# Kernel optimization log

Measured on AMD Instinct MI355X. Metric: run time of the kernel, lower is better.

## Reference

```python
import jax, jax.numpy as jnp
import numpy as np

B, S, HID, NH = 4, 4096, 1024, 16
D = HID // NH                 # head_dim = 64
WIN, CHUNK = 512, 128
CPW = WIN // CHUNK            # chunks_per_window = 4
NW = S // WIN                 # num windows = 8
NC = S // CHUNK               # num chunks = 32
SCALE = D ** -0.5             # head_dim_scaling


def setup_inputs() -> dict:
    key = jax.random.key(0)
    k = jax.random.split(key, 8)
    hidden_states = jax.random.normal(k[0], (B, S, HID), jnp.float32)
    init = lambda kk: jax.random.normal(kk, (HID, HID), jnp.float32) * (HID ** -0.5)
    Wq, Wk, Wv, Wo = init(k[1]), init(k[2]), init(k[3]), init(k[4])
    # nn.Parameter(randn(1,H,1,1,D).clamp(-1,1) * head_dim_scaling)
    adaptive_mu_k = jnp.clip(jax.random.normal(k[5], (1, NH, 1, 1, D), jnp.float32), -1.0, 1.0) * SCALE
    adaptive_phi = jnp.clip(jax.random.normal(k[6], (1, NH, 1, 1, D), jnp.float32), -1.0, 1.0) * SCALE
    # RoPE tables, (1,1,S,D) to broadcast against (B,H,S,D)
    inv_freq = 1.0 / (10000.0 ** (jnp.arange(0, D, 2, dtype=jnp.float32) / D))
    freqs = jnp.einsum('s,f->sf', jnp.arange(S, dtype=jnp.float32), inv_freq)
    emb = jnp.concatenate([freqs, freqs], axis=-1)  # (S, D)
    cos = jnp.cos(emb)[None, None]
    sin = jnp.sin(emb)[None, None]
    return dict(hidden_states=hidden_states, Wq=Wq, Wk=Wk, Wv=Wv, Wo=Wo,
                adaptive_mu_k=adaptive_mu_k, adaptive_phi=adaptive_phi, cos=cos, sin=sin)


def rotate_half(x):
    x1, x2 = jnp.split(x, 2, axis=-1)
    return jnp.concatenate([-x2, x1], axis=-1)


def reference(hidden_states, Wq, Wk, Wv, Wv_unused=None, **_ignored):
    raise NotImplementedError  # replaced below


def _eva_forward(hidden_states, Wq, Wk, Wv, Wo, adaptive_mu_k, adaptive_phi, cos, sin):
    b, s, _ = hidden_states.shape
    def proj(W):  # nn.Linear(bias=False): x @ W.T, then (b,s,H,D)->(b,H,s,D)
        return jnp.einsum('bse,de->bsd', hidden_states, W).reshape(b, s, NH, D).transpose(0, 2, 1, 3)
    q, kt, v = proj(Wq), proj(Wk), proj(Wv)
    q = q * cos + rotate_half(q) * sin
    kt = kt * cos + rotate_half(kt) * sin

    # ---- eva_prep_kv_func: per-chunk control-variate summaries ----
    kc = kt.reshape(b, NH, NC, CHUNK, D)
    vc = v.reshape(b, NH, NC, CHUNK, D)
    mu = adaptive_mu_k.reshape(NH, D)
    phi = adaptive_phi.reshape(NH, D)
    # prm-projection logits: scale*<param,k> - scale*||k||^2/2
    norm = SCALE * 0.5 * jnp.sum(kc * kc, axis=-1)                      # (b,h,c,j)
    beta = jax.nn.softmax(SCALE * jnp.einsum('bhcjd,hd->bhcj', kc, mu) - norm, axis=-1)
    gamma = jax.nn.softmax(SCALE * jnp.einsum('bhcjd,hd->bhcj', kc, phi) - norm, axis=-1)
    rfa_k = jnp.einsum('bhcj,bhcjd->bhcd', beta, kc)                    # (b,h,NC,D)
    rfa_v = jnp.einsum('bhcj,bhcjd->bhcd', gamma, vc)

    # ---- eva_agg_func: windowed exact attn + chunk-RFA attn, joint softmax ----
    qw = q.reshape(b, NH, NW, WIN, D)
    kw = kt.reshape(b, NH, NW, WIN, D)
    vw = v.reshape(b, NH, NW, WIN, D)
    win_scores = SCALE * jnp.einsum('bhwid,bhwjd->bhwij', qw, kw)
    neg = jnp.finfo(win_scores.dtype).min
    causal = jnp.tril(jnp.ones((WIN, WIN), bool))
    win_scores = jnp.where(causal[None, None, None], win_scores, neg)
    chunk_scores = SCALE * jnp.einsum('bhwid,bhcd->bhwic', qw, rfa_k)
    # queries in window w attend to chunk-RFAs of strictly earlier windows
    chunk_ok = (jnp.arange(NC)[None, :] // CPW) < jnp.arange(NW)[:, None]  # (NW,NC)
    chunk_scores = jnp.where(chunk_ok[None, None, :, None, :], chunk_scores, neg)
    attn = jax.nn.softmax(jnp.concatenate([win_scores, chunk_scores], axis=-1), axis=-1)
    out = (jnp.einsum('bhwij,bhwjd->bhwid', attn[..., :WIN], vw)
           + jnp.einsum('bhwic,bhcd->bhwid', attn[..., WIN:], rfa_v))
    out = out.reshape(b, NH, s, D).transpose(0, 2, 1, 3).reshape(b, s, HID)
    return jnp.einsum('bsd,ed->bse', out, Wo)  # o_proj


def reference(hidden_states, Wq, Wk, Wv, Wo, adaptive_mu_k, adaptive_phi, cos, sin):
    return _eva_forward(hidden_states, Wq, Wk, Wv, Wo, adaptive_mu_k, adaptive_phi, cos, sin)
```

## Files before the change

kernel.cpp:

```cpp
#include <hip/hip_runtime.h>
#include <hip/hip_bf16.h>
#include <stdint.h>

#define SCALE_ 0.125f
#define K_L2E 0.18033688f

typedef __bf16 bf16x8 __attribute__((ext_vector_type(8)));
typedef float f32x4 __attribute__((ext_vector_type(4)));
typedef unsigned short us8v __attribute__((ext_vector_type(8)));
typedef unsigned int u32x2 __attribute__((ext_vector_type(2)));

__device__ __forceinline__ unsigned short f2bf(float f) {
  unsigned int u = __builtin_bit_cast(unsigned int, f);
  u += 0x7fffu + ((u >> 16) & 1u);
  return (unsigned short)(u >> 16);
}
__device__ __forceinline__ float bf2f(unsigned short h) {
  unsigned int u = ((unsigned int)h) << 16;
  return __builtin_bit_cast(float, u);
}
__device__ __forceinline__ unsigned short f2bf_n(float f) {
  __bf16 b = (__bf16)f;
  return __builtin_bit_cast(unsigned short, b);
}
__device__ __forceinline__ unsigned packbf(float lo, float hi) {
  return (unsigned)f2bf_n(lo) | ((unsigned)f2bf_n(hi) << 16);
}
__device__ __forceinline__ float exp2_fast(float x) {
  return __builtin_amdgcn_exp2f(x);
}
__device__ __forceinline__ f32x4 mfma16(bf16x8 a, bf16x8 b, f32x4 c) {
  return __builtin_amdgcn_mfma_f32_16x16x32_bf16(a, b, c, 0, 0, 0);
}
__device__ __forceinline__ f32x4 max4(f32x4 a, f32x4 b) {
  f32x4 r;
  r[0] = fmaxf(a[0], b[0]); r[1] = fmaxf(a[1], b[1]);
  r[2] = fmaxf(a[2], b[2]); r[3] = fmaxf(a[3], b[3]);
  return r;
}
__device__ __forceinline__ void gl2lds16(const unsigned short* g, unsigned short* l) {
  __builtin_amdgcn_global_load_lds(
      (const __attribute__((address_space(1))) unsigned int*)g,
      (__attribute__((address_space(3))) unsigned int*)l, 16, 0, 0);
}

__global__ __launch_bounds__(256) void cvt_kernel(const float* __restrict__ src,
                                                  unsigned short* __restrict__ dst,
                                                  int n8) {
  int i = blockIdx.x * 256 + threadIdx.x;
  if (i >= n8) return;
  us8v o;
#pragma unroll
  for (int e = 0; e < 8; ++e) o[e] = f2bf(src[(size_t)i * 8 + e]);
  *(us8v*)(dst + (size_t)i * 8) = o;
}

template <int MODE>
__global__ __launch_bounds__(256, 2) void gemm_kernel(
    const unsigned short* __restrict__ A, const unsigned short* __restrict__ W0,
    const unsigned short* __restrict__ W1, const unsigned short* __restrict__ W2,
    unsigned short* __restrict__ Qb, unsigned short* __restrict__ Kb,
    unsigned short* __restrict__ VT, const float* __restrict__ cosT,
    const float* __restrict__ sinT, float* __restrict__ Out) {
  __shared__ unsigned short As[128 * 32];
  __shared__ unsigned short Bs[128 * 32];
  const int tid = threadIdx.x;
  const int lane = tid & 63, wv = tid >> 6;
  const int lr = lane & 15, lg = lane >> 4;
  const int wr = wv >> 1, wc = wv & 1;
  const int tm = blockIdx.x * 16 + (blockIdx.y >> 3);
  const int tn = blockIdx.y & 7;
  const int z = blockIdx.z;
  const unsigned short* Wp = (MODE == 1) ? W0 : (z == 0 ? W0 : (z == 1 ? W1 : W2));
  const unsigned short* Ab = A + (size_t)tm * 128 * 1024;
  const unsigned short* Wb = Wp + (size_t)tn * 128 * 1024;

  const int srow = tid >> 2;
  const int scol = (tid & 3) * 8;

  f32x4 zero = {0.f, 0.f, 0.f, 0.f};
  f32x4 acc[4][4];
#pragma unroll
  for (int i = 0; i < 4; ++i)
#pragma unroll
    for (int j = 0; j < 4; ++j) acc[i][j] = zero;

  for (int ks = 0; ks < 32; ++ks) {
    const int k0 = ks * 32;
    __syncthreads();
    gl2lds16(Ab + (size_t)srow * 1024 + k0 + scol, As + srow * 32 + scol);
    gl2lds16(Ab + (size_t)(64 + srow) * 1024 + k0 + scol, As + (64 + srow) * 32 + scol);
    gl2lds16(Wb + (size_t)srow * 1024 + k0 + scol, Bs + srow * 32 + scol);
    gl2lds16(Wb + (size_t)(64 + srow) * 1024 + k0 + scol, Bs + (64 + srow) * 32 + scol);
    __syncthreads();
    bf16x8 av[4], bv[4];
#pragma unroll
    for (int mt = 0; mt < 4; ++mt)
      av[mt] = *(const bf16x8*)(As + (wr * 64 + mt * 16 + lr) * 32 + lg * 8);
#pragma unroll
    for (int nt = 0; nt < 4; ++nt)
      bv[nt] = *(const bf16x8*)(Bs + (wc * 64 + nt * 16 + lr) * 32 + lg * 8);
    __builtin_amdgcn_s_setprio(1);
#pragma unroll
    for (int mt = 0; mt < 4; ++mt)
#pragma unroll
      for (int nt = 0; nt < 4; ++nt)
        acc[mt][nt] = mfma16(av[mt], bv[nt], acc[mt][nt]);
    __builtin_amdgcn_s_setprio(0);
  }

  if constexpr (MODE == 0) {
    if (z < 2) {
      unsigned short* Dst = (z == 0) ? Qb : Kb;
#pragma unroll
      for (int mt = 0; mt < 4; ++mt) {
#pragma unroll
        for (int r = 0; r < 4; ++r) {
          const int m = tm * 128 + wr * 64 + mt * 16 + lg * 4 + r;
          const int b = m >> 12, s = m & 4095;
#pragma unroll
          for (int nt = 0; nt < 4; ++nt) {
            const int n = tn * 128 + wc * 64 + nt * 16 + lr;
            const int h = n >> 6, d = n & 63;
            float v = acc[mt][nt][r];
            const float cs = cosT[s * 64 + d];
            const float sn = sinT[s * 64 + d];
            const float pv = acc[mt][nt ^ 2][r];
            v = v * cs + ((nt < 2) ? -pv : pv) * sn;
            Dst[((size_t)(b * 16 + h) * 4096 + s) * 64 + d] = f2bf_n(v);
          }
        }
      }
    } else {
#pragma unroll
      for (int mt = 0; mt < 4; ++mt) {
        const int m0 = tm * 128 + wr * 64 + mt * 16 + lg * 4;
        const int b = m0 >> 12, s0 = m0 & 4095;
#pragma unroll
        for (int nt = 0; nt < 4; ++nt) {
          const int n = tn * 128 + wc * 64 + nt * 16 + lr;
          const int h = n >> 6, d = n & 63;
          u32x2 pw;
          pw[0] = packbf(acc[mt][nt][0], acc[mt][nt][1]);
          pw[1] = packbf(acc[mt][nt][2], acc[mt][nt][3]);
          *(u32x2*)(VT + ((size_t)(b * 16 + h) * 64 + d) * 4096 + s0) = pw;
        }
      }
    }
  } else {
#pragma unroll
    for (int mt = 0; mt < 4; ++mt) {
#pragma unroll
      for (int r = 0; r < 4; ++r) {
        const int m = tm * 128 + wr * 64 + mt * 16 + lg * 4 + r;
#pragma unroll
        for (int nt = 0; nt < 4; ++nt) {
          const int n = tn * 128 + wc * 64 + nt * 16 + lr;
          Out[(size_t)m * 1024 + n] = acc[mt][nt][r];
        }
      }
    }
  }
}

__global__ __launch_bounds__(128) void prep_kernel(
    const unsigned short* __restrict__ Kb, const unsigned short* __restrict__ VT,
    const float* __restrict__ mu, const float* __restrict__ phi,
    unsigned short* __restrict__ rfaK, unsigned short* __restrict__ rfaVT) {
  __shared__ float kc[128][65];
  __shared__ float betaS[128], gammaS[128];
  __shared__ float red[8];
  const int tid = threadIdx.x, lane = tid & 63, wid = tid >> 6;
  const int bh = blockIdx.x >> 5, c = blockIdx.x & 31;
  const int h = bh & 15;
  const size_t rowbase = ((size_t)bh * 4096 + c * 128 + tid) * 64;

  float nn = 0.f, dmu = 0.f, dphi = 0.f;
#pragma unroll
  for (int d8 = 0; d8 < 8; ++d8) {
    us8v kv = *(const us8v*)(Kb + rowbase + d8 * 8);
#pragma unroll
    for (int e = 0; e < 8; ++e) {
      const int d = d8 * 8 + e;
      const float kf = bf2f(kv[e]);
      kc[tid][d] = kf;
      nn += kf * kf;
      dmu += kf * mu[h * 64 + d];
      dphi += kf * phi[h * 64 + d];
    }
  }
  const float lb = SCALE_ * dmu - 0.5f * SCALE_ * nn;
  const float lgm = SCALE_ * dphi - 0.5f * SCALE_ * nn;
  float mb = lb, mg = lgm;
  for (int off = 1; off < 64; off <<= 1) {
    mb = fmaxf(mb, __shfl_xor(mb, off));
    mg = fmaxf(mg, __shfl_xor(mg, off));
  }
  if (lane == 0) { red[wid * 2] = mb; red[wid * 2 + 1] = mg; }
  __syncthreads();
  mb = fmaxf(red[0], red[2]);
  mg = fmaxf(red[1], red[3]);
  const float eb = __expf(lb - mb), eg = __expf(lgm - mg);
  float sb = eb, sg = eg;
  for (int off = 1; off < 64; off <<= 1) {
    sb += __shfl_xor(sb, off);
    sg += __shfl_xor(sg, off);
  }
  if (lane == 0) { red[4 + wid * 2] = sb; red[4 + wid * 2 + 1] = sg; }
  betaS[tid] = eb;
  gammaS[tid] = eg;
  __syncthreads();
  sb = red[4] + red[6];
  sg = red[5] + red[7];

  if (tid < 64) {
    float a = 0.f;
    for (int j = 0; j < 128; ++j) a += betaS[j] * kc[j][tid];
    rfaK[((size_t)bh * 32 + c) * 64 + tid] = f2bf(a / sb);
    const unsigned short* vrow = VT + ((size_t)bh * 64 + tid) * 4096 + c * 128;
    float av = 0.f;
#pragma unroll
    for (int j8 = 0; j8 < 16; ++j8) {
      us8v vv = *(const us8v*)(vrow + j8 * 8);
#pragma unroll
      for (int e = 0; e < 8; ++e) av += gammaS[j8 * 8 + e] * bf2f(vv[e]);
    }
    rfaVT[((size_t)bh * 64 + tid) * 32 + c] = f2bf(av / sg);
  }
}

template <int NCT, bool HASA, bool MASKA, bool MASKB, bool CH>
__device__ __forceinline__ void attn_tile2(
    const unsigned short* __restrict__ ksrc, const unsigned short* __restrict__ vsrc,
    int t, int w, int qrA, int qrB, int lr, int lg, const bf16x8* qaA,
    const bf16x8* qaB, f32x4* oA, f32x4* oB, float& mA, float& lA, float& mB,
    float& lB, unsigned short (*__restrict__ PtA)[136],
    unsigned short (*__restrict__ PtB)[136]) {
  constexpr int VSTRIDE = CH ? 32 : 4096;
  constexpr int NKS = CH ? 1 : 4;
  bf16x8 vf[NKS * 4];
#pragma unroll
  for (int ks = 0; ks < NKS; ++ks)
#pragma unroll
    for (int dt = 0; dt < 4; ++dt)
      vf[ks * 4 + dt] =
          *(const bf16x8*)(vsrc + (size_t)(dt * 16) * VSTRIDE + ks * 32);
  f32x4 stA[NCT], stB[NCT];
#pragma unroll
  for (int ct = 0; ct < NCT; ++ct) {
    bf16x8 b0 = *(const bf16x8*)(ksrc + (ct * 16 + lr) * 64 + lg * 8);
    bf16x8 b1 = *(const bf16x8*)(ksrc + (ct * 16 + lr) * 64 + 32 + lg * 8);
    f32x4 sb_ = {0.f, 0.f, 0.f, 0.f};
    sb_ = mfma16(b0, qaB[0], sb_);
    sb_ = mfma16(b1, qaB[1], sb_);
    f32x4 sa_ = {0.f, 0.f, 0.f, 0.f};
    if constexpr (HASA) {
      sa_ = mfma16(b0, qaA[0], sa_);
      sa_ = mfma16(b1, qaA[1], sa_);
    }
#pragma unroll
    for (int r = 0; r < 4; ++r) {
      const int kidx = ct * 16 + lg * 4 + r;
      float svb = sb_[r] * K_L2E;
      if constexpr (CH) {
        if (kidx >= 4 * w) svb = -1e30f;
      } else if constexpr (MASKB) {
        if (t * 128 + kidx > qrB) svb = -1e30f;
      }
      sb_[r] = svb;
      if constexpr (HASA) {
        float sva = sa_[r] * K_L2E;
        if constexpr (CH) {
          if (kidx >= 4 * w) sva = -1e30f;
        } else if constexpr (MASKA) {
          if (t * 128 + kidx > qrA) sva = -1e30f;
        }
        sa_[r] = sva;
      }
    }
    stB[ct] = sb_;
    if constexpr (HASA) stA[ct] = sa_;
  }
  if constexpr (HASA) {
    f32x4 m4 = stA[0];
#pragma unroll
    for (int ct = 1; ct < NCT; ++ct) m4 = max4(m4, stA[ct]);
    float rm = fmaxf(fmaxf(m4[0], m4[1]), fmaxf(m4[2], m4[3]));
    rm = fmaxf(rm, __shfl_xor(rm, 16));
    rm = fmaxf(rm, __shfl_xor(rm, 32));
    const float mn = fmaxf(mA, rm);
    const float a = exp2_fast(mA - mn);
    f32x4 s4 = {0.f, 0.f, 0.f, 0.f};
#pragma unroll
    for (int ct = 0; ct < NCT; ++ct) {
#pragma unroll
      for (int r = 0; r < 4; ++r) stA[ct][r] = exp2_fast(stA[ct][r] - mn);
      s4 += stA[ct];
    }
    float rs = (s4[0] + s4[1]) + (s4[2] + s4[3]);
    rs += __shfl_xor(rs, 16);
    rs += __shfl_xor(rs, 32);
    lA = lA * a + rs;
    mA = mn;
#pragma unroll
    for (int dt = 0; dt < 4; ++dt)
#pragma unroll
      for (int r = 0; r < 4; ++r) oA[dt][r] *= a;
#pragma unroll
    for (int ct = 0; ct < NCT; ++ct) {
      u32x2 pw;
      pw[0] = packbf(stA[ct][0], stA[ct][1]);
      pw[1] = packbf(stA[ct][2], stA[ct][3]);
      *(u32x2*)&PtA[lr][ct * 16 + lg * 4] = pw;
    }
  }
  {
    f32x4 m4 = stB[0];
#pragma unroll
    for (int ct = 1; ct < NCT; ++ct) m4 = max4(m4, stB[ct]);
    float rm = fmaxf(fmaxf(m4[0], m4[1]), fmaxf(m4[2], m4[3]));
    rm = fmaxf(rm, __shfl_xor(rm, 16));
    rm = fmaxf(rm, __shfl_xor(rm, 32));
    const float mn = fmaxf(mB, rm);
    const float a = exp2_fast(mB - mn);
    f32x4 s4 = {0.f, 0.f, 0.f, 0.f};
#pragma unroll
    for (int ct = 0; ct < NCT; ++ct) {
#pragma unroll
      for (int r = 0; r < 4; ++r) stB[ct][r] = exp2_fast(stB[ct][r] - mn);
      s4 += stB[ct];
    }
    float rs = (s4[0] + s4[1]) + (s4[2] + s4[3]);
    rs += __shfl_xor(rs, 16);
    rs += __shfl_xor(rs, 32);
    lB = lB * a + rs;
    mB = mn;
#pragma unroll
    for (int dt = 0; dt < 4; ++dt)
#pragma unroll
      for (int r = 0; r < 4; ++r) oB[dt][r] *= a;
#pragma unroll
    for (int ct = 0; ct < NCT; ++ct) {
      u32x2 pw;
      pw[0] = packbf(stB[ct][0], stB[ct][1]);
      pw[1] = packbf(stB[ct][2], stB[ct][3]);
      *(u32x2*)&PtB[lr][ct * 16 + lg * 4] = pw;
    }
  }
  asm volatile("s_waitcnt lgkmcnt(0)" ::: "memory");
  __builtin_amdgcn_s_setprio(1);
#pragma unroll
  for (int ks = 0; ks < NKS; ++ks) {
    if constexpr (HASA) {
      bf16x8 pfA = *(const bf16x8*)&PtA[lr][ks * 32 + lg * 8];
#pragma unroll
      for (int dt = 0; dt < 4; ++dt)
        oA[dt] = mfma16(vf[ks * 4 + dt], pfA, oA[dt]);
    }
    bf16x8 pfB = *(const bf16x8*)&PtB[lr][ks * 32 + lg * 8];
#pragma unroll
    for (int dt = 0; dt < 4; ++dt)
      oB[dt] = mfma16(vf[ks * 4 + dt], pfB, oB[dt]);
  }
  __builtin_amdgcn_s_setprio(0);
}

__global__ __launch_bounds__(256, 2) void attn_kernel(
    const unsigned short* __restrict__ Qb, const unsigned short* __restrict__ Kb,
    const unsigned short* __restrict__ VT, const unsigned short* __restrict__ rfaK,
    const unsigned short* __restrict__ rfaVT, unsigned short* __restrict__ AO) {
  __shared__ unsigned short Pt[4][2][16][136];
  const int tid = threadIdx.x, lane = tid & 63, wv = tid >> 6;
  const int lr = lane & 15, lg = lane >> 4;
  const int orig = (blockIdx.x & 7) * 256 + (blockIdx.x >> 3);
  const int p = orig & 3, w = (orig >> 2) & 7, bh = orig >> 5;
  const size_t headbase = (size_t)bh * 4096 * 64;
  const int b = bh >> 4, h = bh & 15;

  const int qtA = p, qtB = 7 - p;
  const int qrA = qtA * 64 + wv * 16 + lr;
  const int qrB = qtB * 64 + wv * 16 + lr;

  bf16x8 qaA[2], qaB[2];
  {
    const size_t qoffA = headbase + (size_t)(w * 512 + qrA) * 64;
    qaA[0] = *(const bf16x8*)(Qb + qoffA + lg * 8);
    qaA[1] = *(const bf16x8*)(Qb + qoffA + 32 + lg * 8);
    const size_t qoffB = headbase + (size_t)(w * 512 + qrB) * 64;
    qaB[0] = *(const bf16x8*)(Qb + qoffB + lg * 8);
    qaB[1] = *(const bf16x8*)(Qb + qoffB + 32 + lg * 8);
  }
  f32x4 oA[4], oB[4];
  float mA = -INFINITY, lA = 0.f, mB = -INFINITY, lB = 0.f;
  {
    f32x4 zero = {0.f, 0.f, 0.f, 0.f};
#pragma unroll
    for (int dt = 0; dt < 4; ++dt) { oA[dt] = zero; oB[dt] = zero; }
  }

  unsigned short(*PtA)[136] = Pt[wv][0];
  unsigned short(*PtB)[136] = Pt[wv][1];
  const unsigned short* vwin =
      VT + ((size_t)bh * 64 + lr) * 4096 + w * 512 + lg * 8;
  const unsigned short* vchk = rfaVT + ((size_t)bh * 64 + lr) * 32 + lg * 8;

  const int nktA = (qtA + 2) >> 1;
  const int nktB = (qtB + 2) >> 1;
  for (int t = 0; t < nktB; ++t) {
    const unsigned short* ksrc = Kb + headbase + (size_t)(w * 512 + t * 128) * 64;
    const unsigned short* vsrc = vwin + t * 128;
    if (t < nktA) {
      if (t == nktA - 1) {
        attn_tile2<8, true, true, false, false>(ksrc, vsrc, t, w, qrA, qrB, lr,
                                                lg, qaA, qaB, oA, oB, mA, lA, mB,
                                                lB, PtA, PtB);
      } else {
        attn_tile2<8, true, false, false, false>(ksrc, vsrc, t, w, qrA, qrB, lr,
                                                 lg, qaA, qaB, oA, oB, mA, lA,
                                                 mB, lB, PtA, PtB);
      }
    } else {
      if (t == nktB - 1) {
        attn_tile2<8, false, false, true, false>(ksrc, vsrc, t, w, qrA, qrB, lr,
                                                 lg, qaA, qaB, oA, oB, mA, lA,
                                                 mB, lB, PtA, PtB);
      } else {
        attn_tile2<8, false, false, false, false>(ksrc, vsrc, t, w, qrA, qrB, lr,
                                                  lg, qaA, qaB, oA, oB, mA, lA,
                                                  mB, lB, PtA, PtB);
      }
    }
  }
  if (w > 0) {
    attn_tile2<2, true, false, false, true>(rfaK + (size_t)bh * 32 * 64, vchk, 0,
                                            w, qrA, qrB, lr, lg, qaA, qaB, oA,
                                            oB, mA, lA, mB, lB, PtA, PtB);
  }

  const int q2 = lane >> 2, db = lane & 3;
  {
    const float inv = 1.0f / lA;
#pragma unroll
    for (int dt = 0; dt < 4; ++dt) {
      u32x2 pw;
      pw[0] = packbf(oA[dt][0] * inv, oA[dt][1] * inv);
      pw[1] = packbf(oA[dt][2] * inv, oA[dt][3] * inv);
      *(u32x2*)&PtA[lr][dt * 16 + lg * 4] = pw;
    }
    const float invb = 1.0f / lB;
#pragma unroll
    for (int dt = 0; dt < 4; ++dt) {
      u32x2 pw;
      pw[0] = packbf(oB[dt][0] * invb, oB[dt][1] * invb);
      pw[1] = packbf(oB[dt][2] * invb, oB[dt][3] * invb);
      *(u32x2*)&PtB[lr][dt * 16 + lg * 4] = pw;
    }
    asm volatile("s_waitcnt lgkmcnt(0)" ::: "memory");
    us8v a0 = *(const us8v*)&PtA[q2][db * 16];
    us8v a1 = *(const us8v*)&PtA[q2][db * 16 + 8];
    const int sA = w * 512 + qtA * 64 + wv * 16 + q2;
    unsigned short* dstA = AO + ((size_t)(b * 4096 + sA)) * 1024 + h * 64 + db * 16;
    *(us8v*)dstA = a0;
    *(us8v*)(dstA + 8) = a1;
    us8v b0 = *(const us8v*)&PtB[q2][db * 16];
    us8v b1 = *(const us8v*)&PtB[q2][db * 16 + 8];
    const int sB = w * 512 + qtB * 64 + wv * 16 + q2;
    unsigned short* dstB = AO + ((size_t)(b * 4096 + sB)) * 1024 + h * 64 + db * 16;
    *(us8v*)dstB = b0;
    *(us8v*)(dstB + 8) = b1;
  }
}

extern "C" void kernel_launch(void* const* d_in, const int* in_sizes, int n_in,
                              void* d_out, int out_size, void* d_ws, size_t ws_size,
                              hipStream_t stream) {
  const float* hidden = (const float*)d_in[0];
  const float* Wq = (const float*)d_in[1];
  const float* Wk = (const float*)d_in[2];
  const float* Wv = (const float*)d_in[3];
  const float* Wo = (const float*)d_in[4];
  const float* mu = (const float*)d_in[5];
  const float* phi = (const float*)d_in[6];
  const float* cosT = (const float*)d_in[7];
  const float* sinT = (const float*)d_in[8];
  float* out = (float*)d_out;

  char* ws = (char*)d_ws;
  unsigned short* hid_bf = (unsigned short*)(ws);
  unsigned short* wq_bf = (unsigned short*)(ws + 33554432);
  unsigned short* wk_bf = (unsigned short*)(ws + 35651584);
  unsigned short* wv_bf = (unsigned short*)(ws + 37748736);
  unsigned short* wo_bf = (unsigned short*)(ws + 39845888);
  unsigned short* Qb = (unsigned short*)(ws + 41943040);
  unsigned short* Kb = (unsigned short*)(ws + 75497472);
  unsigned short* VT = (unsigned short*)(ws + 109051904);
  unsigned short* ao_bf = (unsigned short*)(ws + 142606336);
  unsigned short* rfaK = (unsigned short*)(ws + 176160768);
  unsigned short* rfaVT = (unsigned short*)(ws + 176422912);

  cvt_kernel<<<8192, 256, 0, stream>>>(hidden, hid_bf, 2097152);
  cvt_kernel<<<512, 256, 0, stream>>>(Wq, wq_bf, 131072);
  cvt_kernel<<<512, 256, 0, stream>>>(Wk, wk_bf, 131072);
  cvt_kernel<<<512, 256, 0, stream>>>(Wv, wv_bf, 131072);
  cvt_kernel<<<512, 256, 0, stream>>>(Wo, wo_bf, 131072);

  gemm_kernel<0><<<dim3(8, 128, 3), 256, 0, stream>>>(
      hid_bf, wq_bf, wk_bf, wv_bf, Qb, Kb, VT, cosT, sinT, nullptr);

  prep_kernel<<<2048, 128, 0, stream>>>(Kb, VT, mu, phi, rfaK, rfaVT);

  attn_kernel<<<2048, 256, 0, stream>>>(Qb, Kb, VT, rfaK, rfaVT, ao_bf);

  gemm_kernel<1><<<dim3(8, 128, 1), 256, 0, stream>>>(
      ao_bf, wo_bf, nullptr, nullptr, nullptr, nullptr, nullptr, nullptr, nullptr,
      out);
}
```

Measured before the change: 356.5 us.

## Fuse Q, K, V projections into one GEMM kernel sharing the A tile

Replaces the three-way blockIdx.z split of the QKV projection with a single kernel in which each block loads the hidden-state tile once and multiplies it against the Wq, Wk and Wv tiles, keeping three accumulator sets. The aim is to stop reading the activation tile three times and to cut the grid to a third. In exchange each block holds 192 accumulator floats per thread, which raises register pressure and may spill or lower occupancy under launch_bounds(256,2). The grid also drops to 1024 blocks, giving less parallelism. The output GEMM is split into its own non-templated kernel.

```diff
diff --git a/kernel.cpp b/kernel.cpp
--- a/kernel.cpp
+++ b/kernel.cpp
@@ -55,13 +55,111 @@
   *(us8v*)(dst + (size_t)i * 8) = o;
 }
 
-template <int MODE>
-__global__ __launch_bounds__(256, 2) void gemm_kernel(
+__global__ __launch_bounds__(256, 2) void gemm_qkv_kernel(
     const unsigned short* __restrict__ A, const unsigned short* __restrict__ W0,
     const unsigned short* __restrict__ W1, const unsigned short* __restrict__ W2,
     unsigned short* __restrict__ Qb, unsigned short* __restrict__ Kb,
     unsigned short* __restrict__ VT, const float* __restrict__ cosT,
-    const float* __restrict__ sinT, float* __restrict__ Out) {
+    const float* __restrict__ sinT) {
+  __shared__ unsigned short As[128 * 32];
+  __shared__ unsigned short Bs[3][128 * 32];
+  const int tid = threadIdx.x;
+  const int lane = tid & 63, wv = tid >> 6;
+  const int lr = lane & 15, lg = lane >> 4;
+  const int wr = wv >> 1, wc = wv & 1;
+  const int tm = blockIdx.x * 16 + (blockIdx.y >> 3);
+  const int tn = blockIdx.y & 7;
+  const unsigned short* Ab = A + (size_t)tm * 128 * 1024;
+  const unsigned short* Wb0 = W0 + (size_t)tn * 128 * 1024;
+  const unsigned short* Wb1 = W1 + (size_t)tn * 128 * 1024;
+  const unsigned short* Wb2 = W2 + (size_t)tn * 128 * 1024;
+
+  const int srow = tid >> 2;
+  const int scol = (tid & 3) * 8;
+
+  f32x4 zero = {0.f, 0.f, 0.f, 0.f};
+  f32x4 acc[3][4][4];
+#pragma unroll
+  for (int z = 0; z < 3; ++z)
+#pragma unroll
+    for (int i = 0; i < 4; ++i)
+#pragma unroll
+      for (int j = 0; j < 4; ++j) acc[z][i][j] = zero;
+
+  for (int ks = 0; ks < 32; ++ks) {
+    const int k0 = ks * 32;
+    __syncthreads();
+    gl2lds16(Ab + (size_t)srow * 1024 + k0 + scol, As + srow * 32 + scol);
+    gl2lds16(Ab + (size_t)(64 + srow) * 1024 + k0 + scol, As + (64 + srow) * 32 + scol);
+    gl2lds16(Wb0 + (size_t)srow * 1024 + k0 + scol, Bs[0] + srow * 32 + scol);
+    gl2lds16(Wb0 + (size_t)(64 + srow) * 1024 + k0 + scol, Bs[0] + (64 + srow) * 32 + scol);
+    gl2lds16(Wb1 + (size_t)srow * 1024 + k0 + scol, Bs[1] + srow * 32 + scol);
+    gl2lds16(Wb1 + (size_t)(64 + srow) * 1024 + k0 + scol, Bs[1] + (64 + srow) * 32 + scol);
+    gl2lds16(Wb2 + (size_t)srow * 1024 + k0 + scol, Bs[2] + srow * 32 + scol);
+    gl2lds16(Wb2 + (size_t)(64 + srow) * 1024 + k0 + scol, Bs[2] + (64 + srow) * 32 + scol);
+    __syncthreads();
+    bf16x8 av[4];
+#pragma unroll
+    for (int mt = 0; mt < 4; ++mt)
+      av[mt] = *(const bf16x8*)(As + (wr * 64 + mt * 16 + lr) * 32 + lg * 8);
+    __builtin_amdgcn_s_setprio(1);
+#pragma unroll
+    for (int z = 0; z < 3; ++z) {
+      bf16x8 bv[4];
+#pragma unroll
+      for (int nt = 0; nt < 4; ++nt)
+        bv[nt] = *(const bf16x8*)(Bs[z] + (wc * 64 + nt * 16 + lr) * 32 + lg * 8);
+#pragma unroll
+      for (int mt = 0; mt < 4; ++mt)
+#pragma unroll
+        for (int nt = 0; nt < 4; ++nt)
+          acc[z][mt][nt] = mfma16(av[mt], bv[nt], acc[z][mt][nt]);
+    }
+    __builtin_amdgcn_s_setprio(0);
+  }
+
+#pragma unroll
+  for (int z = 0; z < 2; ++z) {
+    unsigned short* Dst = (z == 0) ? Qb : Kb;
+#pragma unroll
+    for (int mt = 0; mt < 4; ++mt) {
+#pragma unroll
+      for (int r = 0; r < 4; ++r) {
+        const int m = tm * 128 + wr * 64 + mt * 16 + lg * 4 + r;
+        const int b = m >> 12, s = m & 4095;
+#pragma unroll
+        for (int nt = 0; nt < 4; ++nt) {
+          const int n = tn * 128 + wc * 64 + nt * 16 + lr;
+          const int h = n >> 6, d = n & 63;
+          float v = acc[z][mt][nt][r];
+          const float cs = cosT[s * 64 + d];
+          const float sn = sinT[s * 64 + d];
+          const float pv = acc[z][mt][nt ^ 2][r];
+          v = v * cs + ((nt < 2) ? -pv : pv) * sn;
+          Dst[((size_t)(b * 16 + h) * 4096 + s) * 64 + d] = f2bf_n(v);
+        }
+      }
+    }
+  }
+#pragma unroll
+  for (int mt = 0; mt < 4; ++mt) {
+    const int m0 = tm * 128 + wr * 64 + mt * 16 + lg * 4;
+    const int b = m0 >> 12, s0 = m0 & 4095;
+#pragma unroll
+    for (int nt = 0; nt < 4; ++nt) {
+      const int n = tn * 128 + wc * 64 + nt * 16 + lr;
+      const int h = n >> 6, d = n & 63;
+      u32x2 pw;
+      pw[0] = packbf(acc[2][mt][nt][0], acc[2][mt][nt][1]);
+      pw[1] = packbf(acc[2][mt][nt][2], acc[2][mt][nt][3]);
+      *(u32x2*)(VT + ((size_t)(b * 16 + h) * 64 + d) * 4096 + s0) = pw;
+    }
+  }
+}
+
+__global__ __launch_bounds__(256, 2) void gemm_o_kernel(
+    const unsigned short* __restrict__ A, const unsigned short* __restrict__ W0,
+    float* __restrict__ Out) {
   __shared__ unsigned short As[128 * 32];
   __shared__ unsigned short Bs[128 * 32];
   const int tid = threadIdx.x;
@@ -70,10 +168,8 @@
   const int wr = wv >> 1, wc = wv & 1;
   const int tm = blockIdx.x * 16 + (blockIdx.y >> 3);
   const int tn = blockIdx.y & 7;
-  const int z = blockIdx.z;
-  const unsigned short* Wp = (MODE == 1) ? W0 : (z == 0 ? W0 : (z == 1 ? W1 : W2));
   const unsigned short* Ab = A + (size_t)tm * 128 * 1024;
-  const unsigned short* Wb = Wp + (size_t)tn * 128 * 1024;
+  const unsigned short* Wb = W0 + (size_t)tn * 128 * 1024;
 
   const int srow = tid >> 2;
   const int scol = (tid & 3) * 8;
@@ -109,55 +205,15 @@
     __builtin_amdgcn_s_setprio(0);
   }
 
-  if constexpr (MODE == 0) {
-    if (z < 2) {
-      unsigned short* Dst = (z == 0) ? Qb : Kb;
-#pragma unroll
-      for (int mt = 0; mt < 4; ++mt) {
-#pragma unroll
-        for (int r = 0; r < 4; ++r) {
-          const int m = tm * 128 + wr * 64 + mt * 16 + lg * 4 + r;
-          const int b = m >> 12, s = m & 4095;
-#pragma unroll
-          for (int nt = 0; nt < 4; ++nt) {
-            const int n = tn * 128 + wc * 64 + nt * 16 + lr;
-            const int h = n >> 6, d = n & 63;
-            float v = acc[mt][nt][r];
-            const float cs = cosT[s * 64 + d];
-            const float sn = sinT[s * 64 + d];
-            const float pv = acc[mt][nt ^ 2][r];
-            v = v * cs + ((nt < 2) ? -pv : pv) * sn;
-            Dst[((size_t)(b * 16 + h) * 4096 + s) * 64 + d] = f2bf_n(v);
-          }
-        }
-      }
-    } else {
-#pragma unroll
-      for (int mt = 0; mt < 4; ++mt) {
-        const int m0 = tm * 128 + wr * 64 + mt * 16 + lg * 4;
-        const int b = m0 >> 12, s0 = m0 & 4095;
-#pragma unroll
-        for (int nt = 0; nt < 4; ++nt) {
-          const int n = tn * 128 + wc * 64 + nt * 16 + lr;
-          const int h = n >> 6, d = n & 63;
-          u32x2 pw;
-          pw[0] = packbf(acc[mt][nt][0], acc[mt][nt][1]);
-          pw[1] = packbf(acc[mt][nt][2], acc[mt][nt][3]);
-          *(u32x2*)(VT + ((size_t)(b * 16 + h) * 64 + d) * 4096 + s0) = pw;
-        }
-      }
-    }
-  } else {
-#pragma unroll
-    for (int mt = 0; mt < 4; ++mt) {
-#pragma unroll
-      for (int r = 0; r < 4; ++r) {
-        const int m = tm * 128 + wr * 64 + mt * 16 + lg * 4 + r;
-#pragma unroll
-        for (int nt = 0; nt < 4; ++nt) {
-          const int n = tn * 128 + wc * 64 + nt * 16 + lr;
-          Out[(size_t)m * 1024 + n] = acc[mt][nt][r];
-        }
+#pragma unroll
+  for (int mt = 0; mt < 4; ++mt) {
+#pragma unroll
+    for (int r = 0; r < 4; ++r) {
+      const int m = tm * 128 + wr * 64 + mt * 16 + lg * 4 + r;
+#pragma unroll
+      for (int nt = 0; nt < 4; ++nt) {
+        const int n = tn * 128 + wc * 64 + nt * 16 + lr;
+        Out[(size_t)m * 1024 + n] = acc[mt][nt][r];
       }
     }
   }
@@ -504,14 +560,12 @@
   cvt_kernel<<<512, 256, 0, stream>>>(Wv, wv_bf, 131072);
   cvt_kernel<<<512, 256, 0, stream>>>(Wo, wo_bf, 131072);
 
-  gemm_kernel<0><<<dim3(8, 128, 3), 256, 0, stream>>>(
-      hid_bf, wq_bf, wk_bf, wv_bf, Qb, Kb, VT, cosT, sinT, nullptr);
+  gemm_qkv_kernel<<<dim3(8, 128), 256, 0, stream>>>(
+      hid_bf, wq_bf, wk_bf, wv_bf, Qb, Kb, VT, cosT, sinT);
 
   prep_kernel<<<2048, 128, 0, stream>>>(Kb, VT, mu, phi, rfaK, rfaVT);
 
   attn_kernel<<<2048, 256, 0, stream>>>(Qb, Kb, VT, rfaK, rfaVT, ao_bf);
 
-  gemm_kernel<1><<<dim3(8, 128, 1), 256, 0, stream>>>(
-      ao_bf, wo_bf, nullptr, nullptr, nullptr, nullptr, nullptr, nullptr, nullptr,
-      out);
-}
+  gemm_o_kernel<<<dim3(8, 128), 256, 0, stream>>>(ao_bf, wo_bf, out);
+}
```

Result: slower. 372.6 us (+4.5%).

## Prefetch next K tile into registers during current attention tile

Applied to the files above, without the earlier changes.

K fragments for the next key tile (or the chunk-RFA keys after the last window tile) are now loaded into a 16-entry register array right after the current tile's QK MFMAs. This is software pipelining: global-load latency for K can overlap the softmax and PV work of the current tile. The cost is roughly 64 extra VGPRs per thread, which may lower occupancy or cause spills.

```diff
diff --git a/kernel.cpp b/kernel.cpp
--- a/kernel.cpp
+++ b/kernel.cpp
@@ -231,7 +231,8 @@
 
 template <int NCT, bool HASA, bool MASKA, bool MASKB, bool CH>
 __device__ __forceinline__ void attn_tile2(
-    const unsigned short* __restrict__ ksrc, const unsigned short* __restrict__ vsrc,
+    bf16x8* __restrict__ kreg, const unsigned short* __restrict__ knext, int nnext,
+    const unsigned short* __restrict__ vsrc,
     int t, int w, int qrA, int qrB, int lr, int lg, const bf16x8* qaA,
     const bf16x8* qaB, f32x4* oA, f32x4* oB, float& mA, float& lA, float& mB,
     float& lB, unsigned short (*__restrict__ PtA)[136],
@@ -248,15 +249,13 @@
   f32x4 stA[NCT], stB[NCT];
 #pragma unroll
   for (int ct = 0; ct < NCT; ++ct) {
-    bf16x8 b0 = *(const bf16x8*)(ksrc + (ct * 16 + lr) * 64 + lg * 8);
-    bf16x8 b1 = *(const bf16x8*)(ksrc + (ct * 16 + lr) * 64 + 32 + lg * 8);
     f32x4 sb_ = {0.f, 0.f, 0.f, 0.f};
-    sb_ = mfma16(b0, qaB[0], sb_);
-    sb_ = mfma16(b1, qaB[1], sb_);
+    sb_ = mfma16(kreg[2 * ct], qaB[0], sb_);
+    sb_ = mfma16(kreg[2 * ct + 1], qaB[1], sb_);
     f32x4 sa_ = {0.f, 0.f, 0.f, 0.f};
     if constexpr (HASA) {
-      sa_ = mfma16(b0, qaA[0], sa_);
-      sa_ = mfma16(b1, qaA[1], sa_);
+      sa_ = mfma16(kreg[2 * ct], qaA[0], sa_);
+      sa_ = mfma16(kreg[2 * ct + 1], qaA[1], sa_);
     }
 #pragma unroll
     for (int r = 0; r < 4; ++r) {
@@ -280,6 +279,19 @@
     }
     stB[ct] = sb_;
     if constexpr (HASA) stA[ct] = sa_;
+  }
+  if (nnext == 8) {
+#pragma unroll
+    for (int ct = 0; ct < 8; ++ct) {
+      kreg[2 * ct] = *(const bf16x8*)(knext + (ct * 16 + lr) * 64 + lg * 8);
+      kreg[2 * ct + 1] = *(const bf16x8*)(knext + (ct * 16 + lr) * 64 + 32 + lg * 8);
+    }
+  } else if (nnext == 2) {
+#pragma unroll
+    for (int ct = 0; ct < 2; ++ct) {
+      kreg[2 * ct] = *(const bf16x8*)(knext + (ct * 16 + lr) * 64 + lg * 8);
+      kreg[2 * ct + 1] = *(const bf16x8*)(knext + (ct * 16 + lr) * 64 + 32 + lg * 8);
+    }
   }
   if constexpr (HASA) {
     f32x4 m4 = stA[0];
@@ -403,38 +415,58 @@
   const unsigned short* vwin =
       VT + ((size_t)bh * 64 + lr) * 4096 + w * 512 + lg * 8;
   const unsigned short* vchk = rfaVT + ((size_t)bh * 64 + lr) * 32 + lg * 8;
+  const unsigned short* kwin = Kb + headbase + (size_t)(w * 512) * 64;
+  const unsigned short* kchk = rfaK + (size_t)bh * 32 * 64;
+
+  bf16x8 kreg[16];
+#pragma unroll
+  for (int ct = 0; ct < 8; ++ct) {
+    kreg[2 * ct] = *(const bf16x8*)(kwin + (ct * 16 + lr) * 64 + lg * 8);
+    kreg[2 * ct + 1] = *(const bf16x8*)(kwin + (ct * 16 + lr) * 64 + 32 + lg * 8);
+  }
 
   const int nktA = (qtA + 2) >> 1;
   const int nktB = (qtB + 2) >> 1;
   for (int t = 0; t < nktB; ++t) {
-    const unsigned short* ksrc = Kb + headbase + (size_t)(w * 512 + t * 128) * 64;
     const unsigned short* vsrc = vwin + t * 128;
+    int nnext;
+    const unsigned short* knext;
+    if (t + 1 < nktB) {
+      nnext = 8;
+      knext = kwin + (size_t)(t + 1) * 128 * 64;
+    } else if (w > 0) {
+      nnext = 2;
+      knext = kchk;
+    } else {
+      nnext = 0;
+      knext = nullptr;
+    }
     if (t < nktA) {
       if (t == nktA - 1) {
-        attn_tile2<8, true, true, false, false>(ksrc, vsrc, t, w, qrA, qrB, lr,
-                                                lg, qaA, qaB, oA, oB, mA, lA, mB,
-                                                lB, PtA, PtB);
+        attn_tile2<8, true, true, false, false>(kreg, knext, nnext, vsrc, t, w,
+                                                qrA, qrB, lr, lg, qaA, qaB, oA,
+                                                oB, mA, lA, mB, lB, PtA, PtB);
       } else {
-        attn_tile2<8, true, false, false, false>(ksrc, vsrc, t, w, qrA, qrB, lr,
-                                                 lg, qaA, qaB, oA, oB, mA, lA,
-                                                 mB, lB, PtA, PtB);
+        attn_tile2<8, true, false, false, false>(kreg, knext, nnext, vsrc, t, w,
+                                                 qrA, qrB, lr, lg, qaA, qaB, oA,
+                                                 oB, mA, lA, mB, lB, PtA, PtB);
       }
     } else {
       if (t == nktB - 1) {
-        attn_tile2<8, false, false, true, false>(ksrc, vsrc, t, w, qrA, qrB, lr,
-                                                 lg, qaA, qaB, oA, oB, mA, lA,
-                                                 mB, lB, PtA, PtB);
+        attn_tile2<8, false, false, true, false>(kreg, knext, nnext, vsrc, t, w,
+                                                 qrA, qrB, lr, lg, qaA, qaB, oA,
+                                                 oB, mA, lA, mB, lB, PtA, PtB);
       } else {
-        attn_tile2<8, false, false, false, false>(ksrc, vsrc, t, w, qrA, qrB, lr,
-                                                  lg, qaA, qaB, oA, oB, mA, lA,
-                                                  mB, lB, PtA, PtB);
+        attn_tile2<8, false, false, false, false>(kreg, knext, nnext, vsrc, t, w,
+                                                  qrA, qrB, lr, lg, qaA, qaB, oA,
+                                                  oB, mA, lA, mB, lB, PtA, PtB);
       }
     }
   }
   if (w > 0) {
-    attn_tile2<2, true, false, false, true>(rfaK + (size_t)bh * 32 * 64, vchk, 0,
-                                            w, qrA, qrB, lr, lg, qaA, qaB, oA,
-                                            oB, mA, lA, mB, lB, PtA, PtB);
+    attn_tile2<2, true, false, false, true>(kreg, nullptr, 0, vchk, 0, w, qrA,
+                                            qrB, lr, lg, qaA, qaB, oA, oB, mA,
+                                            lA, mB, lB, PtA, PtB);
   }
 
   const int q2 = lane >> 2, db = lane & 3;
```

Measured after the change: 492.9 us. 1.38x slower.

## Stage K tiles through double-buffered swizzled LDS with async global-to-LDS loads

Applied to the files above, without the earlier changes.

K tiles for the window attention, and the chunk-RFA keys, are now loaded cooperatively into a double-buffered shared-memory array with async global-to-LDS copies, and the next tile is prefetched while the current one is computed. Previously each wave read K directly from global memory. The P-tile scratch buffers drop their padding and use an XOR swizzle to avoid bank conflicts. In exchange the loop gains a block-wide barrier per tile and uses more LDS, which could lower occupancy at two blocks per CU.

```diff
diff --git a/kernel.cpp b/kernel.cpp
--- a/kernel.cpp
+++ b/kernel.cpp
@@ -231,13 +231,14 @@
 
 template <int NCT, bool HASA, bool MASKA, bool MASKB, bool CH>
 __device__ __forceinline__ void attn_tile2(
-    const unsigned short* __restrict__ ksrc, const unsigned short* __restrict__ vsrc,
+    const unsigned short* __restrict__ klds, const unsigned short* __restrict__ vsrc,
     int t, int w, int qrA, int qrB, int lr, int lg, const bf16x8* qaA,
     const bf16x8* qaB, f32x4* oA, f32x4* oB, float& mA, float& lA, float& mB,
-    float& lB, unsigned short (*__restrict__ PtA)[136],
-    unsigned short (*__restrict__ PtB)[136]) {
+    float& lB, unsigned short (*__restrict__ PtA)[128],
+    unsigned short (*__restrict__ PtB)[128]) {
   constexpr int VSTRIDE = CH ? 32 : 4096;
   constexpr int NKS = CH ? 1 : 4;
+  const int sw = lr & 7;
   bf16x8 vf[NKS * 4];
 #pragma unroll
   for (int ks = 0; ks < NKS; ++ks)
@@ -248,8 +249,8 @@
   f32x4 stA[NCT], stB[NCT];
 #pragma unroll
   for (int ct = 0; ct < NCT; ++ct) {
-    bf16x8 b0 = *(const bf16x8*)(ksrc + (ct * 16 + lr) * 64 + lg * 8);
-    bf16x8 b1 = *(const bf16x8*)(ksrc + (ct * 16 + lr) * 64 + 32 + lg * 8);
+    bf16x8 b0 = *(const bf16x8*)(klds + (ct * 16 + lr) * 64 + ((lg ^ sw) * 8));
+    bf16x8 b1 = *(const bf16x8*)(klds + (ct * 16 + lr) * 64 + (((4 + lg) ^ sw) * 8));
     f32x4 sb_ = {0.f, 0.f, 0.f, 0.f};
     sb_ = mfma16(b0, qaB[0], sb_);
     sb_ = mfma16(b1, qaB[1], sb_);
@@ -311,7 +312,7 @@
       u32x2 pw;
       pw[0] = packbf(stA[ct][0], stA[ct][1]);
       pw[1] = packbf(stA[ct][2], stA[ct][3]);
-      *(u32x2*)&PtA[lr][ct * 16 + lg * 4] = pw;
+      *(u32x2*)&PtA[lr][((2 * ct + (lg >> 1)) ^ sw) * 8 + (lg & 1) * 4] = pw;
     }
   }
   {
@@ -344,7 +345,7 @@
       u32x2 pw;
       pw[0] = packbf(stB[ct][0], stB[ct][1]);
       pw[1] = packbf(stB[ct][2], stB[ct][3]);
-      *(u32x2*)&PtB[lr][ct * 16 + lg * 4] = pw;
+      *(u32x2*)&PtB[lr][((2 * ct + (lg >> 1)) ^ sw) * 8 + (lg & 1) * 4] = pw;
     }
   }
   asm volatile("s_waitcnt lgkmcnt(0)" ::: "memory");
@@ -352,12 +353,12 @@
 #pragma unroll
   for (int ks = 0; ks < NKS; ++ks) {
     if constexpr (HASA) {
-      bf16x8 pfA = *(const bf16x8*)&PtA[lr][ks * 32 + lg * 8];
+      bf16x8 pfA = *(const bf16x8*)&PtA[lr][((ks * 4 + lg) ^ sw) * 8];
 #pragma unroll
       for (int dt = 0; dt < 4; ++dt)
         oA[dt] = mfma16(vf[ks * 4 + dt], pfA, oA[dt]);
     }
-    bf16x8 pfB = *(const bf16x8*)&PtB[lr][ks * 32 + lg * 8];
+    bf16x8 pfB = *(const bf16x8*)&PtB[lr][((ks * 4 + lg) ^ sw) * 8];
 #pragma unroll
     for (int dt = 0; dt < 4; ++dt)
       oB[dt] = mfma16(vf[ks * 4 + dt], pfB, oB[dt]);
@@ -369,7 +370,8 @@
     const unsigned short* __restrict__ Qb, const unsigned short* __restrict__ Kb,
     const unsigned short* __restrict__ VT, const unsigned short* __restrict__ rfaK,
     const unsigned short* __restrict__ rfaVT, unsigned short* __restrict__ AO) {
-  __shared__ unsigned short Pt[4][2][16][136];
+  __shared__ unsigned short Klds[2][128][64];
+  __shared__ unsigned short Pt[4][2][16][128];
   const int tid = threadIdx.x, lane = tid & 63, wv = tid >> 6;
   const int lr = lane & 15, lg = lane >> 4;
   const int orig = (blockIdx.x & 7) * 256 + (blockIdx.x >> 3);
@@ -398,46 +400,73 @@
     for (int dt = 0; dt < 4; ++dt) { oA[dt] = zero; oB[dt] = zero; }
   }
 
-  unsigned short(*PtA)[136] = Pt[wv][0];
-  unsigned short(*PtB)[136] = Pt[wv][1];
+  unsigned short(*PtA)[128] = Pt[wv][0];
+  unsigned short(*PtB)[128] = Pt[wv][1];
   const unsigned short* vwin =
       VT + ((size_t)bh * 64 + lr) * 4096 + w * 512 + lg * 8;
   const unsigned short* vchk = rfaVT + ((size_t)bh * 64 + lr) * 32 + lg * 8;
+  const unsigned short* kwin = Kb + headbase + (size_t)(w * 512) * 64;
+  const unsigned short* kchk = rfaK + (size_t)bh * 32 * 64;
+
+  auto stage_win = [&](const unsigned short* src, int buf) {
+#pragma unroll
+    for (int i = 0; i < 4; ++i) {
+      const int row = wv * 32 + i * 8 + (lane >> 3);
+      gl2lds16(src + row * 64 + (((lane & 7) ^ (row & 7)) * 8),
+               &Klds[buf][wv * 32 + i * 8][0] + lane * 8);
+    }
+  };
+  auto stage_chk = [&](int buf) {
+    const int row = wv * 8 + (lane >> 3);
+    gl2lds16(kchk + row * 64 + (((lane & 7) ^ (row & 7)) * 8),
+             &Klds[buf][wv * 8][0] + lane * 8);
+  };
 
   const int nktA = (qtA + 2) >> 1;
   const int nktB = (qtB + 2) >> 1;
+
+  stage_win(kwin, 0);
+
   for (int t = 0; t < nktB; ++t) {
-    const unsigned short* ksrc = Kb + headbase + (size_t)(w * 512 + t * 128) * 64;
+    __syncthreads();
+    if (t + 1 < nktB) {
+      stage_win(kwin + (size_t)(t + 1) * 128 * 64, (t + 1) & 1);
+    } else if (w > 0) {
+      stage_chk((t + 1) & 1);
+    }
+    const unsigned short* klds = &Klds[t & 1][0][0];
     const unsigned short* vsrc = vwin + t * 128;
     if (t < nktA) {
       if (t == nktA - 1) {
-        attn_tile2<8, true, true, false, false>(ksrc, vsrc, t, w, qrA, qrB, lr,
+        attn_tile2<8, true, true, false, false>(klds, vsrc, t, w, qrA, qrB, lr,
                                                 lg, qaA, qaB, oA, oB, mA, lA, mB,
                                                 lB, PtA, PtB);
       } else {
-        attn_tile2<8, true, false, false, false>(ksrc, vsrc, t, w, qrA, qrB, lr,
+        attn_tile2<8, true, false, false, false>(klds, vsrc, t, w, qrA, qrB, lr,
                                                  lg, qaA, qaB, oA, oB, mA, lA,
                                                  mB, lB, PtA, PtB);
       }
     } else {
       if (t == nktB - 1) {
-        attn_tile2<8, false, false, true, false>(ksrc, vsrc, t, w, qrA, qrB, lr,
+        attn_tile2<8, false, false, true, false>(klds, vsrc, t, w, qrA, qrB, lr,
                                                  lg, qaA, qaB, oA, oB, mA, lA,
                                                  mB, lB, PtA, PtB);
       } else {
-        attn_tile2<8, false, false, false, false>(ksrc, vsrc, t, w, qrA, qrB, lr,
+        attn_tile2<8, false, false, false, false>(klds, vsrc, t, w, qrA, qrB, lr,
                                                   lg, qaA, qaB, oA, oB, mA, lA,
                                                   mB, lB, PtA, PtB);
       }
     }
   }
   if (w > 0) {
-    attn_tile2<2, true, false, false, true>(rfaK + (size_t)bh * 32 * 64, vchk, 0,
-                                            w, qrA, qrB, lr, lg, qaA, qaB, oA,
-                                            oB, mA, lA, mB, lB, PtA, PtB);
+    __syncthreads();
+    attn_tile2<2, true, false, false, true>(&Klds[nktB & 1][0][0], vchk, 0, w,
+                                            qrA, qrB, lr, lg, qaA, qaB, oA, oB,
+                                            mA, lA, mB, lB, PtA, PtB);
   }
 
   const int q2 = lane >> 2, db = lane & 3;
+  const int sw = lr & 7;
   {
     const float inv = 1.0f / lA;
 #pragma unroll
@@ -445,7 +474,7 @@
       u32x2 pw;
       pw[0] = packbf(oA[dt][0] * inv, oA[dt][1] * inv);
       pw[1] = packbf(oA[dt][2] * inv, oA[dt][3] * inv);
-      *(u32x2*)&PtA[lr][dt * 16 + lg * 4] = pw;
+      *(u32x2*)&PtA[lr][((2 * dt + (lg >> 1)) ^ sw) * 8 + (lg & 1) * 4] = pw;
     }
     const float invb = 1.0f / lB;
 #pragma unroll
@@ -453,17 +482,18 @@
       u32x2 pw;
       pw[0] = packbf(oB[dt][0] * invb, oB[dt][1] * invb);
       pw[1] = packbf(oB[dt][2] * invb, oB[dt][3] * invb);
-      *(u32x2*)&PtB[lr][dt * 16 + lg * 4] = pw;
+      *(u32x2*)&PtB[lr][((2 * dt + (lg >> 1)) ^ sw) * 8 + (lg & 1) * 4] = pw;
     }
     asm volatile("s_waitcnt lgkmcnt(0)" ::: "memory");
-    us8v a0 = *(const us8v*)&PtA[q2][db * 16];
-    us8v a1 = *(const us8v*)&PtA[q2][db * 16 + 8];
+    const int swq = q2 & 7;
+    us8v a0 = *(const us8v*)&PtA[q2][((2 * db) ^ swq) * 8];
+    us8v a1 = *(const us8v*)&PtA[q2][((2 * db + 1) ^ swq) * 8];
     const int sA = w * 512 + qtA * 64 + wv * 16 + q2;
     unsigned short* dstA = AO + ((size_t)(b * 4096 + sA)) * 1024 + h * 64 + db * 16;
     *(us8v*)dstA = a0;
     *(us8v*)(dstA + 8) = a1;
-    us8v b0 = *(const us8v*)&PtB[q2][db * 16];
-    us8v b1 = *(const us8v*)&PtB[q2][db * 16 + 8];
+    us8v b0 = *(const us8v*)&PtB[q2][((2 * db) ^ swq) * 8];
+    us8v b1 = *(const us8v*)&PtB[q2][((2 * db + 1) ^ swq) * 8];
     const int sB = w * 512 + qtB * 64 + wv * 16 + q2;
     unsigned short* dstB = AO + ((size_t)(b * 4096 + sB)) * 1024 + h * 64 + db * 16;
     *(us8v*)dstB = b0;
```

New measurement: 334.7 us. -6.1%, faster.
